# Kernel optimization log

Hardware: AMD Instinct MI355X
Metric: run time of the kernel (lower is better)

The kernel has to match this reference:

```python
import jax, jax.numpy as jnp
import numpy as np
import math

B, S, D, H = 4, 2048, 512, 8
HD = D // H

def setup_inputs() -> dict:
    key = jax.random.key(0)
    ks = jax.random.split(key, 12)
    s_hd = 1.0 / math.sqrt(HD)
    s_d = 1.0 / math.sqrt(D)
    return {
        "q": jax.random.normal(ks[0], (B, S, D), jnp.float32),
        "k": jax.random.normal(ks[1], (B, S, D), jnp.float32),
        "v": jax.random.normal(ks[2], (B, S, D), jnp.float32),
        # torch nn.Linear(head_dim, head_dim): weight [HD, HD], bias [HD]
        "Wq": jax.random.uniform(ks[3], (HD, HD), jnp.float32, -s_hd, s_hd),
        "bq": jax.random.uniform(ks[4], (HD,), jnp.float32, -s_hd, s_hd),
        "Wk": jax.random.uniform(ks[5], (HD, HD), jnp.float32, -s_hd, s_hd),
        "bk": jax.random.uniform(ks[6], (HD,), jnp.float32, -s_hd, s_hd),
        "Wv": jax.random.uniform(ks[7], (HD, HD), jnp.float32, -s_hd, s_hd),
        "bv": jax.random.uniform(ks[8], (HD,), jnp.float32, -s_hd, s_hd),
        # output projection nn.Linear(d, d)
        "Wo": jax.random.uniform(ks[9], (D, D), jnp.float32, -s_d, s_d),
        "bo": jax.random.uniform(ks[10], (D,), jnp.float32, -s_d, s_d),
        # LayerNorm(d) affine params
        "gamma": jnp.ones((D,), jnp.float32),
        "beta": jnp.zeros((D,), jnp.float32),
    }

def _layernorm(x, gamma, beta, eps=1e-5):
    mu = jnp.mean(x, axis=-1, keepdims=True)
    var = jnp.var(x, axis=-1, keepdims=True)
    return (x - mu) * jax.lax.rsqrt(var + eps) * gamma + beta

def reference(q, k, v, Wq, bq, Wk, bk, Wv, bv, Wo, bo, gamma, beta):
    batch, q_len = q.shape[0], q.shape[1]
    # split heads: [B, L, H, HD]; per-head Linear shares one weight across heads
    Qh = q.reshape(batch, q_len, H, HD) @ Wq.T + bq
    Kh = k.reshape(batch, k.shape[1], H, HD) @ Wk.T + bk
    Vh = v.reshape(batch, v.shape[1], H, HD) @ Wv.T + bv
    # scores scaled by sqrt(d) (faithful to source, NOT sqrt(head_dim))
    scores = jnp.einsum('bqhd,bkhd->bhqk', Qh, Kh) / math.sqrt(D)
    attn = jax.nn.softmax(scores, axis=-1)
    out = jnp.einsum('bhqk,bkhd->bqhd', attn, Vh)
    concat = out.reshape(batch, q_len, D)
    lin = concat @ Wo.T + bo
    # AddNorm quirk: residual added AFTER LayerNorm (dropout = identity in eval)
    return q + _layernorm(lin, gamma, beta)
```

## Files before the change

kernel.cpp:

```cpp
#include <hip/hip_runtime.h>
#include <hip/hip_bf16.h>
#include <math.h>
#include <stdint.h>

#define B 4
#define S 2048
#define D 512
#define H 8
#define HD 64

typedef __attribute__((ext_vector_type(4))) int   int4v;
typedef __attribute__((ext_vector_type(8))) short short8;
typedef __attribute__((ext_vector_type(4))) short short4v;
typedef __attribute__((ext_vector_type(4))) float f32x4;

__device__ __forceinline__ unsigned short bfr(float x) {
    __bf16 h = (__bf16)x;
    union { __bf16 b; unsigned short s; } u; u.b = h; return u.s;
}
__device__ __forceinline__ float ex2(float x) { return exp2f(x); }

#define QSCALE 0.06377229601488305f
#define MFIX 4.0f

typedef const __attribute__((address_space(1))) unsigned char g8_t;
typedef __attribute__((address_space(3))) unsigned char l8_t;
__device__ __forceinline__ void gl_lds16(const unsigned short* g, unsigned short* l) {
#if __has_builtin(__builtin_amdgcn_global_load_lds)
    __builtin_amdgcn_global_load_lds((g8_t*)g, (l8_t*)l, 16, 0, 0);
#else
    int lane = threadIdx.x & 63;
    ((int4v*)l)[lane] = *(const int4v*)g;
#endif
}

__global__ __launch_bounds__(256) void wcvt_kernel(
    const float* __restrict__ Wo, const float* __restrict__ Wq,
    const float* __restrict__ Wk, const float* __restrict__ Wv,
    unsigned short* __restrict__ WoB, unsigned short* __restrict__ WqB,
    unsigned short* __restrict__ WkB, unsigned short* __restrict__ WvB)
{
    int bid = blockIdx.x;
    const float* src; unsigned short* dst; int base;
    if (bid < 256)      { src = Wo; dst = WoB; base = bid * 1024; }
    else if (bid < 260) { src = Wq; dst = WqB; base = (bid - 256) * 1024; }
    else if (bid < 264) { src = Wk; dst = WkB; base = (bid - 260) * 1024; }
    else                { src = Wv; dst = WvB; base = (bid - 264) * 1024; }
    int i = base + threadIdx.x * 4;
    float4 f = *(const float4*)(src + i);
    short4v s;
    s[0] = (short)bfr(f.x); s[1] = (short)bfr(f.y);
    s[2] = (short)bfr(f.z); s[3] = (short)bfr(f.w);
    *(short4v*)(dst + i) = s;
}

__global__ __launch_bounds__(256) void qkv_mfma_kernel(
    const float* __restrict__ q, const float* __restrict__ k,
    const float* __restrict__ v,
    const unsigned short* __restrict__ WqB, const float* __restrict__ bq,
    const unsigned short* __restrict__ WkB, const float* __restrict__ bk,
    const unsigned short* __restrict__ WvB, const float* __restrict__ bv,
    unsigned short* __restrict__ Qh, unsigned short* __restrict__ Kh,
    unsigned short* __restrict__ VtG)
{
    const int t = threadIdx.x;
    const int L = t & 63, w = t >> 6;
    const int c = L & 15, qd = L >> 4;
    const int task = blockIdx.x * 4 + w;
    const int st = task & 127;
    const int h  = (task >> 7) & 7;
    const int b  = (task >> 10) & 3;
    const int x  = task >> 12;

    const unsigned short* WB = (x == 0) ? WqB : (x == 1) ? WkB : WvB;
    const float* bias_p      = (x == 0) ? bq  : (x == 1) ? bk  : bv;
    const float* X           = (x == 0) ? q   : (x == 1) ? k   : v;

    const float* xrow = X + ((size_t)(b * S + st * 16 + c)) * D + h * HD;
    short8 af[2];
    #pragma unroll
    for (int kc = 0; kc < 2; ++kc) {
        float4 f0 = *(const float4*)(xrow + kc * 32 + 8 * qd);
        float4 f1 = *(const float4*)(xrow + kc * 32 + 8 * qd + 4);
        short8 s8;
        s8[0] = (short)bfr(f0.x); s8[1] = (short)bfr(f0.y);
        s8[2] = (short)bfr(f0.z); s8[3] = (short)bfr(f0.w);
        s8[4] = (short)bfr(f1.x); s8[5] = (short)bfr(f1.y);
        s8[6] = (short)bfr(f1.z); s8[7] = (short)bfr(f1.w);
        af[kc] = s8;
    }

    if (x < 2) {
        f32x4 acc[4];
        #pragma unroll
        for (int nt = 0; nt < 4; ++nt) {
            float bv_ = bias_p[16 * nt + c];
            acc[nt] = (f32x4){bv_, bv_, bv_, bv_};
            short8 b0 = *(const short8*)(WB + (16 * nt + c) * HD + 8 * qd);
            short8 b1 = *(const short8*)(WB + (16 * nt + c) * HD + 32 + 8 * qd);
            acc[nt] = __builtin_amdgcn_mfma_f32_16x16x32_bf16(af[0], b0, acc[nt], 0, 0, 0);
            acc[nt] = __builtin_amdgcn_mfma_f32_16x16x32_bf16(af[1], b1, acc[nt], 0, 0, 0);
        }
        unsigned short* O = ((x == 0) ? Qh : Kh)
                          + ((size_t)(b * H + h) * S + st * 16) * HD;
        const float sc = (x == 0) ? QSCALE : 1.0f;
        #pragma unroll
        for (int nt = 0; nt < 4; ++nt)
            #pragma unroll
            for (int r = 0; r < 4; ++r)
                O[(4 * qd + r) * HD + 16 * nt + c] = bfr(acc[nt][r] * sc);
    } else {
        f32x4 acc[4];
        #pragma unroll
        for (int nt = 0; nt < 4; ++nt) {
            float4 bb4 = *(const float4*)(bias_p + 16 * nt + 4 * qd);
            acc[nt] = (f32x4){bb4.x, bb4.y, bb4.z, bb4.w};
            short8 a0 = *(const short8*)(WB + (16 * nt + c) * HD + 8 * qd);
            short8 a1 = *(const short8*)(WB + (16 * nt + c) * HD + 32 + 8 * qd);
            acc[nt] = __builtin_amdgcn_mfma_f32_16x16x32_bf16(a0, af[0], acc[nt], 0, 0, 0);
            acc[nt] = __builtin_amdgcn_mfma_f32_16x16x32_bf16(a1, af[1], acc[nt], 0, 0, 0);
        }
        unsigned short* O = VtG + (size_t)(b * H + h) * HD * S;
        #pragma unroll
        for (int nt = 0; nt < 4; ++nt)
            #pragma unroll
            for (int r = 0; r < 4; ++r)
                O[(size_t)(16 * nt + 4 * qd + r) * S + st * 16 + c] = bfr(acc[nt][r]);
    }
}

__global__ __launch_bounds__(256, 4) void attn_kernel(
    const unsigned short* __restrict__ Qh, const unsigned short* __restrict__ Kh,
    const unsigned short* __restrict__ VtG, float* __restrict__ accP,
    float* __restrict__ lP)
{
    __shared__ __align__(16) unsigned short Ks[2][4096];
    __shared__ __align__(16) unsigned short Vs[2][4096];

    const int idx = blockIdx.x;
    const int bh = idx >> 5;
    const int rem = idx & 31;
    const int qt = rem >> 1;
    const int ks = rem & 1;
    const int b = bh >> 3, h = bh & 7;
    const int t = threadIdx.x;
    const int w = t >> 6, L = t & 63;
    const int c = L & 15, qd = L >> 4;

    const unsigned short* Kb = Kh + ((size_t)bh * S + ks * 1024) * HD;
    const unsigned short* Vb = VtG + (size_t)bh * HD * S + ks * 1024;

    short8 qf[2][2];
    #pragma unroll
    for (int qg = 0; qg < 2; ++qg)
        #pragma unroll
        for (int kc = 0; kc < 2; ++kc)
            qf[qg][kc] = *(const short8*)(Qh
                + ((size_t)bh * S + qt * 128 + w * 32 + qg * 16 + c) * HD
                + kc * 32 + 8 * qd);

    f32x4 acc[2][4];
    float lrun[2] = {0.f, 0.f};
    #pragma unroll
    for (int qg = 0; qg < 2; ++qg)
        #pragma unroll
        for (int dt = 0; dt < 4; ++dt) acc[qg][dt] = (f32x4){0.f, 0.f, 0.f, 0.f};

    const int sd = t >> 3, sj = t & 7;
    const int sp = sj >> 2, smt = (sj >> 1) & 1;
    const int sqa = (2 * sj) & 3, sqb = (2 * sj + 1) & 3;

    int4v vpre[2];
    #pragma unroll
    for (int i = 0; i < 2; ++i) {
        int bi = w + 4 * i;
        gl_lds16(Kb + (size_t)(16 * (bi >> 1) + c) * HD + (bi & 1) * 32 + qd * 8,
                 &Ks[0][bi * 512]);
        vpre[i] = *(const int4v*)(Vb + (size_t)(sd + 32 * i) * S + 8 * sj);
    }

    for (int it = 0; it < 16; ++it) {
        const int cur = it & 1, nxt = cur ^ 1;
        #pragma unroll
        for (int i = 0; i < 2; ++i) {
            int d = sd + 32 * i;
            int dt = d >> 4, cc = d & 15;
            union { int4v v; short4v h[2]; } u; u.v = vpre[i];
            *(short4v*)&Vs[cur][((dt * 2 + sp) * 64 + sqa * 16 + cc) * 8 + smt * 4] = u.h[0];
            *(short4v*)&Vs[cur][((dt * 2 + sp) * 64 + sqb * 16 + cc) * 8 + smt * 4] = u.h[1];
        }
        __syncthreads();
        if (it + 1 < 16) {
            int n1 = (it + 1) * 64;
            #pragma unroll
            for (int i = 0; i < 2; ++i) {
                int bi = w + 4 * i;
                gl_lds16(Kb + (size_t)(n1 + 16 * (bi >> 1) + c) * HD + (bi & 1) * 32 + qd * 8,
                         &Ks[nxt][bi * 512]);
                vpre[i] = *(const int4v*)(Vb + (size_t)(sd + 32 * i) * S + n1 + 8 * sj);
            }
        }

        const unsigned short* KsC = Ks[cur];
        const unsigned short* VsC = Vs[cur];

        short4v pa[2][4];
        #pragma unroll
        for (int mt = 0; mt < 4; ++mt) {
            short8 a0 = *(const short8*)(KsC + (mt * 2 + 0) * 512 + L * 8);
            short8 a1 = *(const short8*)(KsC + (mt * 2 + 1) * 512 + L * 8);
            #pragma unroll
            for (int qg = 0; qg < 2; ++qg) {
                f32x4 stv = (f32x4){-MFIX, -MFIX, -MFIX, -MFIX};
                stv = __builtin_amdgcn_mfma_f32_16x16x32_bf16(a0, qf[qg][0], stv, 0, 0, 0);
                stv = __builtin_amdgcn_mfma_f32_16x16x32_bf16(a1, qf[qg][1], stv, 0, 0, 0);
                float p0 = ex2(stv[0]), p1 = ex2(stv[1]);
                float p2 = ex2(stv[2]), p3 = ex2(stv[3]);
                lrun[qg] += (p0 + p1) + (p2 + p3);
                short4v p_;
                p_[0] = (short)bfr(p0); p_[1] = (short)bfr(p1);
                p_[2] = (short)bfr(p2); p_[3] = (short)bfr(p3);
                pa[qg][mt] = p_;
            }
        }

        #pragma unroll
        for (int dt = 0; dt < 4; ++dt)
            #pragma unroll
            for (int p = 0; p < 2; ++p) {
                union { short8 v8; short4v h[2]; } u;
                u.v8 = *(const short8*)(VsC + (dt * 2 + p) * 512 + L * 8);
#if __has_builtin(__builtin_amdgcn_mfma_f32_16x16x16bf16_1k)
                #pragma unroll
                for (int qg = 0; qg < 2; ++qg) {
                    acc[qg][dt] = __builtin_amdgcn_mfma_f32_16x16x16bf16_1k(
                        pa[qg][2 * p + 0], u.h[0], acc[qg][dt], 0, 0, 0);
                    acc[qg][dt] = __builtin_amdgcn_mfma_f32_16x16x16bf16_1k(
                        pa[qg][2 * p + 1], u.h[1], acc[qg][dt], 0, 0, 0);
                }
#else
                #pragma unroll
                for (int qg = 0; qg < 2; ++qg) {
                    short8 pz0 = {pa[qg][2 * p + 0][0], pa[qg][2 * p + 0][1],
                                  pa[qg][2 * p + 0][2], pa[qg][2 * p + 0][3], 0, 0, 0, 0};
                    short8 pz1 = {pa[qg][2 * p + 1][0], pa[qg][2 * p + 1][1],
                                  pa[qg][2 * p + 1][2], pa[qg][2 * p + 1][3], 0, 0, 0, 0};
                    short8 v0 = {u.h[0][0], u.h[0][1], u.h[0][2], u.h[0][3], 0, 0, 0, 0};
                    short8 v1 = {u.h[1][0], u.h[1][1], u.h[1][2], u.h[1][3], 0, 0, 0, 0};
                    acc[qg][dt] = __builtin_amdgcn_mfma_f32_16x16x32_bf16(pz0, v0, acc[qg][dt], 0, 0, 0);
                    acc[qg][dt] = __builtin_amdgcn_mfma_f32_16x16x32_bf16(pz1, v1, acc[qg][dt], 0, 0, 0);
                }
#endif
            }
    }

    const int q0 = qt * 128 + w * 32;
    float* accPp = accP + (size_t)ks * ((size_t)B * S * D)
                 + ((size_t)b * S + q0) * D + h * HD;
    #pragma unroll
    for (int qg = 0; qg < 2; ++qg) {
        float lr = lrun[qg];
        lr += __shfl_xor(lr, 16);
        lr += __shfl_xor(lr, 32);
        if (qd == 0)
            lP[(size_t)ks * ((size_t)B * H * S) + (size_t)bh * S + q0 + qg * 16 + c] = lr;
        #pragma unroll
        for (int dt = 0; dt < 4; ++dt)
            #pragma unroll
            for (int r = 0; r < 4; ++r)
                accPp[(size_t)(qg * 16 + 4 * qd + r) * D + 16 * dt + c] = acc[qg][dt][r];
    }
}

__global__ __launch_bounds__(256) void oproj_ln_kernel(
    const float* __restrict__ accP, const float* __restrict__ lP,
    const unsigned short* __restrict__ WoB,
    const float* __restrict__ bo, const float* __restrict__ gamma,
    const float* __restrict__ beta, const float* __restrict__ qin,
    float* __restrict__ out)
{
    __shared__ __align__(16) unsigned short As[32 * 520];
    __shared__ float red[2][4][32];
    __shared__ float linv_s[32][8];

    const int t = threadIdx.x;
    const int r0 = blockIdx.x * 32;
    const int w = t >> 6, L = t & 63;
    const int c = L & 15, qd = L >> 4;
    const int n0 = w * 128;
    const size_t NEf = (size_t)B * S * D;
    const size_t BHS = (size_t)B * H * S;

    {
        int row = t >> 3, hh = t & 7;
        int bb = r0 >> 11;
        int ss = (r0 & (S - 1)) + row;
        float l0 = lP[(size_t)(bb * H + hh) * S + ss];
        float l1 = lP[BHS + (size_t)(bb * H + hh) * S + ss];
        linv_s[row][hh] = 1.f / (l0 + l1);
    }
    __syncthreads();

    #pragma unroll
    for (int i = 0; i < 16; ++i) {
        int flat = t + 256 * i;
        int row = flat >> 7, cg = flat & 127;
        int col = cg * 4;
        size_t gi = (size_t)(r0 + row) * D + col;
        float4 a0 = *(const float4*)(accP + gi);
        float4 a1 = *(const float4*)(accP + NEf + gi);
        float li = linv_s[row][col >> 6];
        short4v s;
        s[0] = (short)bfr((a0.x + a1.x) * li);
        s[1] = (short)bfr((a0.y + a1.y) * li);
        s[2] = (short)bfr((a0.z + a1.z) * li);
        s[3] = (short)bfr((a0.w + a1.w) * li);
        *(short4v*)&As[row * 520 + col] = s;
    }
    __syncthreads();

    f32x4 acc[2][8];
    #pragma unroll
    for (int nt = 0; nt < 8; ++nt) {
        float bv_ = bo[n0 + 16 * nt + c];
        acc[0][nt] = (f32x4){bv_, bv_, bv_, bv_};
        acc[1][nt] = (f32x4){bv_, bv_, bv_, bv_};
    }

    for (int kc = 0; kc < 16; ++kc) {
        short8 a0 = *(const short8*)&As[c * 520 + kc * 32 + 8 * qd];
        short8 a1 = *(const short8*)&As[(16 + c) * 520 + kc * 32 + 8 * qd];
        #pragma unroll
        for (int nt = 0; nt < 8; ++nt) {
            short8 bf = *(const short8*)(WoB + (size_t)(n0 + 16 * nt + c) * D
                                         + kc * 32 + 8 * qd);
            acc[0][nt] = __builtin_amdgcn_mfma_f32_16x16x32_bf16(a0, bf, acc[0][nt], 0, 0, 0);
            acc[1][nt] = __builtin_amdgcn_mfma_f32_16x16x32_bf16(a1, bf, acc[1][nt], 0, 0, 0);
        }
    }

    float sm[2][4], sq[2][4];
    #pragma unroll
    for (int mt = 0; mt < 2; ++mt)
        #pragma unroll
        for (int r = 0; r < 4; ++r) { sm[mt][r] = 0.f; sq[mt][r] = 0.f; }
    #pragma unroll
    for (int mt = 0; mt < 2; ++mt)
        #pragma unroll
        for (int nt = 0; nt < 8; ++nt)
            #pragma unroll
            for (int r = 0; r < 4; ++r) {
                float x_ = acc[mt][nt][r];
                sm[mt][r] += x_; sq[mt][r] += x_ * x_;
            }
    #pragma unroll
    for (int mask = 1; mask <= 8; mask <<= 1)
        #pragma unroll
        for (int mt = 0; mt < 2; ++mt)
            #pragma unroll
            for (int r = 0; r < 4; ++r) {
                sm[mt][r] += __shfl_xor(sm[mt][r], mask);
                sq[mt][r] += __shfl_xor(sq[mt][r], mask);
            }
    if (c == 0) {
        #pragma unroll
        for (int mt = 0; mt < 2; ++mt)
            #pragma unroll
            for (int r = 0; r < 4; ++r) {
                red[0][w][16 * mt + 4 * qd + r] = sm[mt][r];
                red[1][w][16 * mt + 4 * qd + r] = sq[mt][r];
            }
    }
    __syncthreads();

    float mu[2][4], rs[2][4];
    #pragma unroll
    for (int mt = 0; mt < 2; ++mt)
        #pragma unroll
        for (int r = 0; r < 4; ++r) {
            int m_ = 16 * mt + 4 * qd + r;
            float s_ = red[0][0][m_] + red[0][1][m_] + red[0][2][m_] + red[0][3][m_];
            float q_ = red[1][0][m_] + red[1][1][m_] + red[1][2][m_] + red[1][3][m_];
            float mu_ = s_ * (1.f / D);
            float var = q_ * (1.f / D) - mu_ * mu_;
            mu[mt][r] = mu_;
            rs[mt][r] = rsqrtf(var + 1e-5f);
        }

    #pragma unroll
    for (int nt = 0; nt < 8; ++nt) {
        int n = n0 + 16 * nt + c;
        float g = gamma[n], be = beta[n];
        #pragma unroll
        for (int mt = 0; mt < 2; ++mt)
            #pragma unroll
            for (int r = 0; r < 4; ++r) {
                size_t gi = (size_t)(r0 + 16 * mt + 4 * qd + r) * D + n;
                out[gi] = qin[gi] + (acc[mt][nt][r] - mu[mt][r]) * rs[mt][r] * g + be;
            }
    }
}

extern "C" void kernel_launch(void* const* d_in, const int* in_sizes, int n_in,
                              void* d_out, int out_size, void* d_ws, size_t ws_size,
                              hipStream_t stream) {
    const float* q     = (const float*)d_in[0];
    const float* k     = (const float*)d_in[1];
    const float* v     = (const float*)d_in[2];
    const float* Wq    = (const float*)d_in[3];
    const float* bq    = (const float*)d_in[4];
    const float* Wk    = (const float*)d_in[5];
    const float* bk    = (const float*)d_in[6];
    const float* Wv    = (const float*)d_in[7];
    const float* bv    = (const float*)d_in[8];
    const float* Wo    = (const float*)d_in[9];
    const float* bo    = (const float*)d_in[10];
    const float* gamma = (const float*)d_in[11];
    const float* beta  = (const float*)d_in[12];
    float* out = (float*)d_out;

    const size_t NE = (size_t)B * S * D;
    unsigned short* wsu = (unsigned short*)d_ws;
    unsigned short* Qh  = wsu;
    unsigned short* Kh  = wsu + NE;
    unsigned short* VtG = wsu + 2 * NE;
    unsigned short* WoB = wsu + 3 * NE;
    unsigned short* WqB = WoB + (size_t)D * D;
    unsigned short* WkB = WqB + HD * HD;
    unsigned short* WvB = WkB + HD * HD;
    float* accP = (float*)(WvB + HD * HD);
    float* lP   = accP + 2 * NE;

    hipLaunchKernelGGL(wcvt_kernel, dim3(268), dim3(256), 0, stream,
                       Wo, Wq, Wk, Wv, WoB, WqB, WkB, WvB);
    hipLaunchKernelGGL(qkv_mfma_kernel, dim3(3072), dim3(256), 0, stream,
                       q, k, v, WqB, bq, WkB, bk, WvB, bv, Qh, Kh, VtG);
    hipLaunchKernelGGL(attn_kernel, dim3(1024), dim3(256), 0, stream,
                       Qh, Kh, VtG, accP, lP);
    hipLaunchKernelGGL(oproj_ln_kernel, dim3(B * S / 32), dim3(256), 0, stream,
                       accP, lP, WoB, bo, gamma, beta, q, out);
}
```

Before: 217.3 us.

## Swizzle V tile in LDS, use native exp2, and retile output projection

Applies an XOR swizzle to the V tile's LDS stores and loads in the attention kernel to reduce bank conflicts, and replaces exp2f with the amdgcn exp2 builtin. The output-projection+LayerNorm kernel now handles 16 rows per block with 512 threads, each wave covering 64 output columns. This doubles the block count and lowers per-thread accumulator registers to raise occupancy. The cost is twice as many reads of the Wo weights from global memory and a reduction across 8 waves instead of 4.

```diff
diff --git a/kernel.cpp b/kernel.cpp
--- a/kernel.cpp
+++ b/kernel.cpp
@@ -18,7 +18,13 @@
     __bf16 h = (__bf16)x;
     union { __bf16 b; unsigned short s; } u; u.b = h; return u.s;
 }
-__device__ __forceinline__ float ex2(float x) { return exp2f(x); }
+__device__ __forceinline__ float ex2(float x) {
+#if __has_builtin(__builtin_amdgcn_exp2f)
+    return __builtin_amdgcn_exp2f(x);
+#else
+    return exp2f(x);
+#endif
+}
 
 #define QSCALE 0.06377229601488305f
 #define MFIX 4.0f
@@ -169,6 +175,7 @@
     const int sd = t >> 3, sj = t & 7;
     const int sp = sj >> 2, smt = (sj >> 1) & 1;
     const int sqa = (2 * sj) & 3, sqb = (2 * sj + 1) & 3;
+    const int sxor = sp << 2;
 
     int4v vpre[2];
     #pragma unroll
@@ -186,8 +193,8 @@
             int d = sd + 32 * i;
             int dt = d >> 4, cc = d & 15;
             union { int4v v; short4v h[2]; } u; u.v = vpre[i];
-            *(short4v*)&Vs[cur][((dt * 2 + sp) * 64 + sqa * 16 + cc) * 8 + smt * 4] = u.h[0];
-            *(short4v*)&Vs[cur][((dt * 2 + sp) * 64 + sqb * 16 + cc) * 8 + smt * 4] = u.h[1];
+            *(short4v*)&Vs[cur][((dt * 2 + sp) * 64 + ((sqa * 16 + cc) ^ sxor)) * 8 + smt * 4] = u.h[0];
+            *(short4v*)&Vs[cur][((dt * 2 + sp) * 64 + ((sqb * 16 + cc) ^ sxor)) * 8 + smt * 4] = u.h[1];
         }
         __syncthreads();
         if (it + 1 < 16) {
@@ -229,7 +236,7 @@
             #pragma unroll
             for (int p = 0; p < 2; ++p) {
                 union { short8 v8; short4v h[2]; } u;
-                u.v8 = *(const short8*)(VsC + (dt * 2 + p) * 512 + L * 8);
+                u.v8 = *(const short8*)(VsC + (dt * 2 + p) * 512 + (L ^ (p << 2)) * 8);
 #if __has_builtin(__builtin_amdgcn_mfma_f32_16x16x16bf16_1k)
                 #pragma unroll
                 for (int qg = 0; qg < 2; ++qg) {
@@ -272,26 +279,26 @@
     }
 }
 
-__global__ __launch_bounds__(256) void oproj_ln_kernel(
+__global__ __launch_bounds__(512) void oproj_ln_kernel(
     const float* __restrict__ accP, const float* __restrict__ lP,
     const unsigned short* __restrict__ WoB,
     const float* __restrict__ bo, const float* __restrict__ gamma,
     const float* __restrict__ beta, const float* __restrict__ qin,
     float* __restrict__ out)
 {
-    __shared__ __align__(16) unsigned short As[32 * 520];
-    __shared__ float red[2][4][32];
-    __shared__ float linv_s[32][8];
+    __shared__ __align__(16) unsigned short As[16 * 520];
+    __shared__ float red[2][8][16];
+    __shared__ float linv_s[16][8];
 
     const int t = threadIdx.x;
-    const int r0 = blockIdx.x * 32;
+    const int r0 = blockIdx.x * 16;
     const int w = t >> 6, L = t & 63;
     const int c = L & 15, qd = L >> 4;
-    const int n0 = w * 128;
+    const int n0 = w * 64;
     const size_t NEf = (size_t)B * S * D;
     const size_t BHS = (size_t)B * H * S;
 
-    {
+    if (t < 128) {
         int row = t >> 3, hh = t & 7;
         int bb = r0 >> 11;
         int ss = (r0 & (S - 1)) + row;
@@ -302,8 +309,8 @@
     __syncthreads();
 
     #pragma unroll
-    for (int i = 0; i < 16; ++i) {
-        int flat = t + 256 * i;
+    for (int i = 0; i < 4; ++i) {
+        int flat = t + 512 * i;
         int row = flat >> 7, cg = flat & 127;
         int col = cg * 4;
         size_t gi = (size_t)(r0 + row) * D + col;
@@ -319,85 +326,71 @@
     }
     __syncthreads();
 
-    f32x4 acc[2][8];
-    #pragma unroll
-    for (int nt = 0; nt < 8; ++nt) {
+    f32x4 acc[4];
+    #pragma unroll
+    for (int nt = 0; nt < 4; ++nt) {
         float bv_ = bo[n0 + 16 * nt + c];
-        acc[0][nt] = (f32x4){bv_, bv_, bv_, bv_};
-        acc[1][nt] = (f32x4){bv_, bv_, bv_, bv_};
+        acc[nt] = (f32x4){bv_, bv_, bv_, bv_};
     }
 
     for (int kc = 0; kc < 16; ++kc) {
         short8 a0 = *(const short8*)&As[c * 520 + kc * 32 + 8 * qd];
-        short8 a1 = *(const short8*)&As[(16 + c) * 520 + kc * 32 + 8 * qd];
-        #pragma unroll
-        for (int nt = 0; nt < 8; ++nt) {
+        #pragma unroll
+        for (int nt = 0; nt < 4; ++nt) {
             short8 bf = *(const short8*)(WoB + (size_t)(n0 + 16 * nt + c) * D
                                          + kc * 32 + 8 * qd);
-            acc[0][nt] = __builtin_amdgcn_mfma_f32_16x16x32_bf16(a0, bf, acc[0][nt], 0, 0, 0);
-            acc[1][nt] = __builtin_amdgcn_mfma_f32_16x16x32_bf16(a1, bf, acc[1][nt], 0, 0, 0);
-        }
-    }
-
-    float sm[2][4], sq[2][4];
-    #pragma unroll
-    for (int mt = 0; mt < 2; ++mt)
-        #pragma unroll
-        for (int r = 0; r < 4; ++r) { sm[mt][r] = 0.f; sq[mt][r] = 0.f; }
-    #pragma unroll
-    for (int mt = 0; mt < 2; ++mt)
-        #pragma unroll
-        for (int nt = 0; nt < 8; ++nt)
-            #pragma unroll
-            for (int r = 0; r < 4; ++r) {
-                float x_ = acc[mt][nt][r];
-                sm[mt][r] += x_; sq[mt][r] += x_ * x_;
-            }
+            acc[nt] = __builtin_amdgcn_mfma_f32_16x16x32_bf16(a0, bf, acc[nt], 0, 0, 0);
+        }
+    }
+
+    float sm[4], sq[4];
+    #pragma unroll
+    for (int r = 0; r < 4; ++r) { sm[r] = 0.f; sq[r] = 0.f; }
+    #pragma unroll
+    for (int nt = 0; nt < 4; ++nt)
+        #pragma unroll
+        for (int r = 0; r < 4; ++r) {
+            float x_ = acc[nt][r];
+            sm[r] += x_; sq[r] += x_ * x_;
+        }
     #pragma unroll
     for (int mask = 1; mask <= 8; mask <<= 1)
         #pragma unroll
-        for (int mt = 0; mt < 2; ++mt)
-            #pragma unroll
-            for (int r = 0; r < 4; ++r) {
-                sm[mt][r] += __shfl_xor(sm[mt][r], mask);
-                sq[mt][r] += __shfl_xor(sq[mt][r], mask);
-            }
+        for (int r = 0; r < 4; ++r) {
+            sm[r] += __shfl_xor(sm[r], mask);
+            sq[r] += __shfl_xor(sq[r], mask);
+        }
     if (c == 0) {
         #pragma unroll
-        for (int mt = 0; mt < 2; ++mt)
-            #pragma unroll
-            for (int r = 0; r < 4; ++r) {
-                red[0][w][16 * mt + 4 * qd + r] = sm[mt][r];
-                red[1][w][16 * mt + 4 * qd + r] = sq[mt][r];
-            }
+        for (int r = 0; r < 4; ++r) {
+            red[0][w][4 * qd + r] = sm[r];
+            red[1][w][4 * qd + r] = sq[r];
+        }
     }
     __syncthreads();
 
-    float mu[2][4], rs[2][4];
-    #pragma unroll
-    for (int mt = 0; mt < 2; ++mt)
-        #pragma unroll
-        for (int r = 0; r < 4; ++r) {
-            int m_ = 16 * mt + 4 * qd + r;
-            float s_ = red[0][0][m_] + red[0][1][m_] + red[0][2][m_] + red[0][3][m_];
-            float q_ = red[1][0][m_] + red[1][1][m_] + red[1][2][m_] + red[1][3][m_];
-            float mu_ = s_ * (1.f / D);
-            float var = q_ * (1.f / D) - mu_ * mu_;
-            mu[mt][r] = mu_;
-            rs[mt][r] = rsqrtf(var + 1e-5f);
-        }
-
-    #pragma unroll
-    for (int nt = 0; nt < 8; ++nt) {
+    float mu[4], rs[4];
+    #pragma unroll
+    for (int r = 0; r < 4; ++r) {
+        int m_ = 4 * qd + r;
+        float s_ = 0.f, q_ = 0.f;
+        #pragma unroll
+        for (int w_ = 0; w_ < 8; ++w_) { s_ += red[0][w_][m_]; q_ += red[1][w_][m_]; }
+        float mu_ = s_ * (1.f / D);
+        float var = q_ * (1.f / D) - mu_ * mu_;
+        mu[r] = mu_;
+        rs[r] = rsqrtf(var + 1e-5f);
+    }
+
+    #pragma unroll
+    for (int nt = 0; nt < 4; ++nt) {
         int n = n0 + 16 * nt + c;
         float g = gamma[n], be = beta[n];
         #pragma unroll
-        for (int mt = 0; mt < 2; ++mt)
-            #pragma unroll
-            for (int r = 0; r < 4; ++r) {
-                size_t gi = (size_t)(r0 + 16 * mt + 4 * qd + r) * D + n;
-                out[gi] = qin[gi] + (acc[mt][nt][r] - mu[mt][r]) * rs[mt][r] * g + be;
-            }
+        for (int r = 0; r < 4; ++r) {
+            size_t gi = (size_t)(r0 + 4 * qd + r) * D + n;
+            out[gi] = qin[gi] + (acc[nt][r] - mu[r]) * rs[r] * g + be;
+        }
     }
 }
 
@@ -437,6 +430,6 @@
                        q, k, v, WqB, bq, WkB, bk, WvB, bv, Qh, Kh, VtG);
     hipLaunchKernelGGL(attn_kernel, dim3(1024), dim3(256), 0, stream,
                        Qh, Kh, VtG, accP, lP);
-    hipLaunchKernelGGL(oproj_ln_kernel, dim3(B * S / 32), dim3(256), 0, stream,
+    hipLaunchKernelGGL(oproj_ln_kernel, dim3(B * S / 16), dim3(512), 0, stream,
                        accP, lP, WoB, bo, gamma, beta, q, out);
 }
```

Result: slower. 237.2 us (+9.2%).
